# Performance work log

Measured on AMD Instinct MI355X. Metric: run time of the kernel, lower is better.

## Reference

```python
import jax, jax.numpy as jnp
import numpy as np

N, E = 100000, 1600000
IN_D, HID, OUT_D = 64, 64, 16
BN_EPS = 1e-5


def setup_inputs() -> dict:
    key = jax.random.key(0)
    ks = list(jax.random.split(key, 32))
    k = iter(ks)
    inp = {}
    inp["x"] = jax.random.normal(next(k), (N, IN_D), dtype=jnp.float32)
    inp["edge_index"] = jax.random.randint(next(k), (2, E), 0, N, dtype=jnp.int64)
    def lin(kk, fan_in, fan_out):
        s = 1.0 / np.sqrt(fan_in)
        return jax.random.uniform(kk, (fan_in, fan_out), jnp.float32, -s, s)
    for i, ind in ((1, IN_D), (2, HID), (3, HID)):
        inp[f"eps{i}"] = jnp.zeros((), jnp.float32)
        inp[f"w{i}1"] = lin(next(k), ind, HID)
        inp[f"b{i}1"] = jnp.zeros((HID,), jnp.float32)
        inp[f"w{i}2"] = lin(next(k), HID, HID)
        inp[f"b{i}2"] = jnp.zeros((HID,), jnp.float32)
        inp[f"g{i}"] = jnp.ones((HID,), jnp.float32)
        inp[f"bt{i}"] = jnp.zeros((HID,), jnp.float32)
    inp["wl"] = lin(next(k), HID, OUT_D)
    inp["bl"] = jnp.zeros((OUT_D,), jnp.float32)
    return inp


def _gin_conv(x, src, dst, eps, w1, b1, w2, b2, g, bt):
    # scatter-add neighbor sum: agg[i] = sum_{(s->i) in E} x[s]
    agg = jax.ops.segment_sum(x[src], dst, num_segments=N)
    h = (1.0 + eps) * x + agg
    h = jax.nn.relu(h @ w1 + b1)
    h = jax.nn.relu(h @ w2 + b2)
    # BatchNorm1d over nodes (training mode: batch stats, biased variance)
    mu = jnp.mean(h, axis=0)
    var = jnp.var(h, axis=0)
    h = (h - mu) * jax.lax.rsqrt(var + BN_EPS) * g + bt
    return h


def reference(x, edge_index,
              eps1, w11, b11, w12, b12, g1, bt1,
              eps2, w21, b21, w22, b22, g2, bt2,
              eps3, w31, b31, w32, b32, g3, bt3,
              wl, bl):
    src, dst = edge_index[0], edge_index[1]
    h = jax.nn.relu(_gin_conv(x, src, dst, eps1, w11, b11, w12, b12, g1, bt1))
    h = jax.nn.relu(_gin_conv(h, src, dst, eps2, w21, b21, w22, b22, g2, bt2))
    h = jax.nn.relu(_gin_conv(h, src, dst, eps3, w31, b31, w32, b32, g3, bt3))
    return h @ wl + bl
```

## Files before the change

kernel.cpp:

```cpp
#include <hip/hip_runtime.h>
#include <hip/hip_fp16.h>
#include <math.h>

#define N_NODES 100000
#define NC 391
#define NBLK64 1563
#define BN_EPS 1e-5f
#define PART_BLOCKS 128

typedef _Float16 half4v __attribute__((ext_vector_type(4)));
typedef float f32x4 __attribute__((ext_vector_type(4)));

__global__ void zero_misc_k(float* stats, int* gcnt) {
    int gid = blockIdx.x * blockDim.x + threadIdx.x;
    if (gid < 384) stats[gid] = 0.f;
    if (gid < NC) gcnt[gid] = 0;
}

__global__ void tofp16_k(const float* __restrict__ x, __half* __restrict__ xh, int n4) {
    int gid = blockIdx.x * blockDim.x + threadIdx.x;
    if (gid >= n4) return;
    float4 v = reinterpret_cast<const float4*>(x)[gid];
    union { float2 f; __half2 h[2]; } u;
    u.h[0] = __float22half2_rn(make_float2(v.x, v.y));
    u.h[1] = __float22half2_rn(make_float2(v.z, v.w));
    reinterpret_cast<float2*>(xh)[gid] = u.f;
}

__global__ void wtr_k(const float* w0, const float* w1, const float* w2,
                      const float* w3, const float* w4, const float* w5,
                      _Float16* wth) {
    const float* src[6] = {w0, w1, w2, w3, w4, w5};
    const float* W = src[blockIdx.x];
    _Float16* D = wth + (size_t)blockIdx.x * 4096;
    for (int idx = threadIdx.x; idx < 4096; idx += 256) {
        int k = idx >> 6, c = idx & 63;
        D[c * 64 + k] = (_Float16)W[idx];
    }
}

__global__ __launch_bounds__(256) void histC_k(const int* __restrict__ ei,
                                               int* __restrict__ gcnt, int E) {
    __shared__ int cnt[NC];
    for (int i = threadIdx.x; i < NC; i += 256) cnt[i] = 0;
    __syncthreads();
    int per = (E + gridDim.x - 1) / gridDim.x;
    int s0 = blockIdx.x * per, s1 = min(E, s0 + per);
    for (int e = s0 + threadIdx.x; e < s1; e += 256)
        atomicAdd(&cnt[ei[E + e] >> 8], 1);
    __syncthreads();
    for (int i = threadIdx.x; i < NC; i += 256)
        if (cnt[i]) atomicAdd(&gcnt[i], cnt[i]);
}

__global__ __launch_bounds__(256) void scanC_k(const int* __restrict__ gcnt,
                                               int* __restrict__ cbase,
                                               int* __restrict__ gcursor) {
    __shared__ int tmp[256];
    int t = threadIdx.x;
    int v0 = (2 * t < NC) ? gcnt[2 * t] : 0;
    int v1 = (2 * t + 1 < NC) ? gcnt[2 * t + 1] : 0;
    int s = v0 + v1;
    tmp[t] = s;
    __syncthreads();
    for (int off = 1; off < 256; off <<= 1) {
        int a = (t >= off) ? tmp[t - off] : 0;
        __syncthreads();
        tmp[t] += a;
        __syncthreads();
    }
    int run = tmp[t] - s;
    if (2 * t < NC) { cbase[2 * t] = run; gcursor[2 * t] = run; }
    run += v0;
    if (2 * t + 1 < NC) { cbase[2 * t + 1] = run; gcursor[2 * t + 1] = run; }
    if (t == 255) cbase[NC] = tmp[255];
}

__global__ __launch_bounds__(256) void partC_k(const int* __restrict__ ei,
                                               int* __restrict__ gcursor,
                                               int* __restrict__ part, int E) {
    __shared__ int cnt[NC];
    __shared__ int base[NC];
    for (int i = threadIdx.x; i < NC; i += 256) cnt[i] = 0;
    __syncthreads();
    int per = (E + gridDim.x - 1) / gridDim.x;
    int s0 = blockIdx.x * per, s1 = min(E, s0 + per);
    for (int e = s0 + threadIdx.x; e < s1; e += 256)
        atomicAdd(&cnt[ei[E + e] >> 8], 1);
    __syncthreads();
    for (int i = threadIdx.x; i < NC; i += 256) {
        int c = cnt[i];
        base[i] = c ? atomicAdd(&gcursor[i], c) : 0;
    }
    __syncthreads();
    for (int i = threadIdx.x; i < NC; i += 256) cnt[i] = 0;
    __syncthreads();
    for (int e = s0 + threadIdx.x; e < s1; e += 256) {
        int s = ei[e], d = ei[E + e];
        int b = d >> 8, dl = d & 255;
        int lo = atomicAdd(&cnt[b], 1);
        part[base[b] + lo] = (dl << 17) | s;
    }
}

__global__ __launch_bounds__(256) void csrD_k(const int* __restrict__ part,
                                              const int* __restrict__ cbase,
                                              int* __restrict__ row_ptr,
                                              int* __restrict__ csr_src) {
    __shared__ int cnt[256];
    __shared__ int tmp[256];
    __shared__ int cur[256];
    int b = blockIdx.x;
    int t = threadIdx.x;
    int e0 = cbase[b], e1 = cbase[b + 1];
    cnt[t] = 0;
    __syncthreads();
    for (int i = e0 + t; i < e1; i += 256) atomicAdd(&cnt[(part[i] >> 17) & 255], 1);
    __syncthreads();
    int c = cnt[t];
    tmp[t] = c;
    __syncthreads();
    for (int off = 1; off < 256; off <<= 1) {
        int a = (t >= off) ? tmp[t - off] : 0;
        __syncthreads();
        tmp[t] += a;
        __syncthreads();
    }
    int excl = tmp[t] - c;
    int node = b * 256 + t;
    if (node < N_NODES) row_ptr[node] = e0 + excl;
    cur[t] = e0 + excl;
    __syncthreads();
    for (int i = e0 + t; i < e1; i += 256) {
        int u = part[i];
        int dl = (u >> 17) & 255;
        int pos = atomicAdd(&cur[dl], 1);
        csr_src[pos] = u & 0x1FFFF;
    }
    if (b == NC - 1 && t == 0) row_ptr[N_NODES] = cbase[NC];
}

__global__ __launch_bounds__(512) void layer_k(
    const __half* __restrict__ hin,
    const int* __restrict__ row_ptr, const int* __restrict__ csr_src,
    const float* __restrict__ epsp,
    const _Float16* __restrict__ wt1, const float* __restrict__ b1,
    const _Float16* __restrict__ wt2, const float* __restrict__ b2,
    __half* __restrict__ hout, float* __restrict__ stats) {
    __shared__ _Float16 xs[64][72];
    __shared__ float sred[128];

    int tid = threadIdx.x;
    int r0 = blockIdx.x * 64;
    if (tid < 128) sred[tid] = 0.f;

    float eps1 = 1.0f + *epsp;
    int cg8 = tid & 7;
    int rloc = tid >> 3;
    union F4H { float4 f; __half2 h[4]; };

    {
        int node = r0 + rloc;
        float acc[8] = {0.f, 0.f, 0.f, 0.f, 0.f, 0.f, 0.f, 0.f};
        if (node < N_NODES) {
            F4H sv;
            sv.f = reinterpret_cast<const float4*>(hin + (size_t)node * 64)[cg8];
#pragma unroll
            for (int p = 0; p < 4; ++p) {
                float2 gg = __half22float2(sv.h[p]);
                acc[2 * p] = gg.x * eps1;
                acc[2 * p + 1] = gg.y * eps1;
            }
            int j0 = row_ptr[node], j1 = row_ptr[node + 1];
            int j = j0;
            for (; j + 8 <= j1; j += 8) {
                int idx[8];
#pragma unroll
                for (int q = 0; q < 8; ++q) idx[q] = csr_src[j + q];
                F4H u[8];
#pragma unroll
                for (int q = 0; q < 8; ++q)
                    u[q].f = reinterpret_cast<const float4*>(hin + (size_t)idx[q] * 64)[cg8];
#pragma unroll
                for (int q = 0; q < 8; ++q) {
#pragma unroll
                    for (int p = 0; p < 4; ++p) {
                        float2 gg = __half22float2(u[q].h[p]);
                        acc[2 * p] += gg.x;
                        acc[2 * p + 1] += gg.y;
                    }
                }
            }
            for (; j + 2 <= j1; j += 2) {
                int ia = csr_src[j], ib = csr_src[j + 1];
                F4H ua, ub;
                ua.f = reinterpret_cast<const float4*>(hin + (size_t)ia * 64)[cg8];
                ub.f = reinterpret_cast<const float4*>(hin + (size_t)ib * 64)[cg8];
#pragma unroll
                for (int p = 0; p < 4; ++p) {
                    float2 ga = __half22float2(ua.h[p]);
                    float2 gb = __half22float2(ub.h[p]);
                    acc[2 * p] += ga.x + gb.x;
                    acc[2 * p + 1] += ga.y + gb.y;
                }
            }
            for (; j < j1; ++j) {
                F4H u;
                u.f = reinterpret_cast<const float4*>(hin + (size_t)csr_src[j] * 64)[cg8];
#pragma unroll
                for (int p = 0; p < 4; ++p) {
                    float2 gg = __half22float2(u.h[p]);
                    acc[2 * p] += gg.x;
                    acc[2 * p + 1] += gg.y;
                }
            }
        }
        F4H o;
#pragma unroll
        for (int p = 0; p < 4; ++p)
            o.h[p] = __float22half2_rn(make_float2(acc[2 * p], acc[2 * p + 1]));
        *reinterpret_cast<float4*>(&xs[rloc][cg8 * 8]) = o.f;
    }
    __syncthreads();

    int wid = tid >> 6, l = tid & 63;
    int strip = wid & 3, half = wid >> 2;
    int c = l & 15, g = l >> 4;
    int r_base = r0 + strip * 16;

    half4v a1[4];
#pragma unroll
    for (int kk = 0; kk < 4; ++kk)
        a1[kk] = *reinterpret_cast<const half4v*>(&xs[strip * 16 + c][g * 4 + kk * 16]);

    f32x4 acc1[2];
#pragma unroll
    for (int nn = 0; nn < 2; ++nn) {
        int n = half * 2 + nn;
        const _Float16* bb = wt1 + (size_t)(n * 16 + c) * 64 + g * 4;
        half4v bf[4];
#pragma unroll
        for (int kk = 0; kk < 4; ++kk)
            bf[kk] = *reinterpret_cast<const half4v*>(bb + kk * 16);
        f32x4 z = {0.f, 0.f, 0.f, 0.f};
#pragma unroll
        for (int kk = 0; kk < 4; ++kk)
            z = __builtin_amdgcn_mfma_f32_16x16x16f16(a1[kk], bf[kk], z, 0, 0, 0);
        acc1[nn] = z;
    }
    __syncthreads();

#pragma unroll
    for (int nn = 0; nn < 2; ++nn) {
        int n = half * 2 + nn;
        float bj = b1[n * 16 + c];
#pragma unroll
        for (int e = 0; e < 4; ++e) {
            float v = fmaxf(acc1[nn][e] + bj, 0.f);
            xs[strip * 16 + g * 4 + e][n * 16 + c] = (_Float16)v;
        }
    }
    __syncthreads();

    half4v a2[4];
#pragma unroll
    for (int kk = 0; kk < 4; ++kk)
        a2[kk] = *reinterpret_cast<const half4v*>(&xs[strip * 16 + c][kk * 16 + g * 4]);

    f32x4 acc2[2];
#pragma unroll
    for (int nn = 0; nn < 2; ++nn) {
        int n = half * 2 + nn;
        const _Float16* bb = wt2 + (size_t)(n * 16 + c) * 64 + g * 4;
        half4v bf[4];
#pragma unroll
        for (int kk = 0; kk < 4; ++kk)
            bf[kk] = *reinterpret_cast<const half4v*>(bb + kk * 16);
        f32x4 z = {0.f, 0.f, 0.f, 0.f};
#pragma unroll
        for (int kk = 0; kk < 4; ++kk)
            z = __builtin_amdgcn_mfma_f32_16x16x16f16(a2[kk], bf[kk], z, 0, 0, 0);
        acc2[nn] = z;
    }
    __syncthreads();

#pragma unroll
    for (int nn = 0; nn < 2; ++nn) {
        int n = half * 2 + nn;
        float bj = b2[n * 16 + c];
        float s = 0.f, q = 0.f;
#pragma unroll
        for (int e = 0; e < 4; ++e) {
            float v = fmaxf(acc2[nn][e] + bj, 0.f);
            xs[strip * 16 + g * 4 + e][n * 16 + c] = (_Float16)v;
            if (r_base + g * 4 + e < N_NODES) { s += v; q += v * v; }
        }
        atomicAdd(&sred[n * 16 + c], s);
        atomicAdd(&sred[64 + n * 16 + c], q);
    }
    __syncthreads();

    {
        int row = wid * 8 + (l >> 3);
        int colh = (l & 7) * 8;
        int grow = r0 + row;
        if (grow < N_NODES) {
            float4 v = *reinterpret_cast<const float4*>(&xs[row][colh]);
            *reinterpret_cast<float4*>(reinterpret_cast<__half*>(hout) +
                                       (size_t)grow * 64 + colh) = v;
        }
    }

    if (tid < 128) atomicAdd(&stats[tid], sred[tid]);
}

__global__ __launch_bounds__(256) void bnrelu_k(const __half* hin,
                                                const float* __restrict__ stats,
                                                const float* __restrict__ g,
                                                const float* __restrict__ bt,
                                                __half* hout) {
    __shared__ float ssc[64], sof[64];
    int tid = threadIdx.x;
    if (tid < 64) {
        float mean = stats[tid] * (1.f / N_NODES);
        float var = stats[64 + tid] * (1.f / N_NODES) - mean * mean;
        float sc = g[tid] * rsqrtf(var + BN_EPS);
        ssc[tid] = sc;
        sof[tid] = bt[tid] - mean * sc;
    }
    __syncthreads();
    int gid = blockIdx.x * 256 + tid;
    if (gid >= N_NODES * 8) return;
    int c0 = (gid & 7) * 8;
    union { float4 f; __half2 h[4]; } u;
    u.f = reinterpret_cast<const float4*>(hin)[gid];
#pragma unroll
    for (int q = 0; q < 4; ++q) {
        float2 v = __half22float2(u.h[q]);
        v.x = fmaxf(fmaf(v.x, ssc[c0 + 2 * q], sof[c0 + 2 * q]), 0.f);
        v.y = fmaxf(fmaf(v.y, ssc[c0 + 2 * q + 1], sof[c0 + 2 * q + 1]), 0.f);
        u.h[q] = __float22half2_rn(v);
    }
    reinterpret_cast<float4*>(hout)[gid] = u.f;
}

__global__ __launch_bounds__(256) void final_k(const __half* __restrict__ hin,
                                               const float* __restrict__ wl,
                                               const float* __restrict__ bl,
                                               float* __restrict__ out) {
    __shared__ float xs[64][68];
    __shared__ float wsh[64 * 16];
    __shared__ float bsh[16];
    int tid = threadIdx.x;
    int r0 = blockIdx.x * 64;

    reinterpret_cast<float4*>(wsh)[tid] = reinterpret_cast<const float4*>(wl)[tid];
    if (tid < 16) bsh[tid] = bl[tid];

    {
        int rr = tid >> 4, cg = tid & 15;
#pragma unroll
        for (int i = 0; i < 4; ++i) {
            int r = rr + i * 16;
            float4 v = make_float4(0.f, 0.f, 0.f, 0.f);
            if (r0 + r < N_NODES) {
                union { float2 f; __half2 h[2]; } u;
                u.f = reinterpret_cast<const float2*>(hin + (size_t)(r0 + r) * 64)[cg];
                float2 f0 = __half22float2(u.h[0]);
                float2 f1 = __half22float2(u.h[1]);
                v = make_float4(f0.x, f0.y, f1.x, f1.y);
            }
            xs[cg * 4 + 0][r] = v.x;
            xs[cg * 4 + 1][r] = v.y;
            xs[cg * 4 + 2][r] = v.z;
            xs[cg * 4 + 3][r] = v.w;
        }
    }
    __syncthreads();

    int tc = tid & 3, r = tid >> 2;
    int c = tc * 4;
    float acc0 = 0.f, acc1 = 0.f, acc2 = 0.f, acc3 = 0.f;
#pragma unroll 8
    for (int k = 0; k < 64; ++k) {
        float xv = xs[k][r];
        float4 wv = *reinterpret_cast<const float4*>(&wsh[k * 16 + c]);
        acc0 = fmaf(xv, wv.x, acc0);
        acc1 = fmaf(xv, wv.y, acc1);
        acc2 = fmaf(xv, wv.z, acc2);
        acc3 = fmaf(xv, wv.w, acc3);
    }
    int row = r0 + r;
    if (row < N_NODES) {
        float4 o = make_float4(acc0 + bsh[c], acc1 + bsh[c + 1], acc2 + bsh[c + 2], acc3 + bsh[c + 3]);
        *reinterpret_cast<float4*>(out + (size_t)row * 16 + c) = o;
    }
}

extern "C" void kernel_launch(void* const* d_in, const int* in_sizes, int n_in,
                              void* d_out, int out_size, void* d_ws, size_t ws_size,
                              hipStream_t stream) {
    const float* x = (const float*)d_in[0];
    const int* ei = (const int*)d_in[1];
    const int E = in_sizes[1] / 2;

    const float* eps[3] = {(const float*)d_in[2], (const float*)d_in[9], (const float*)d_in[16]};
    const float* w1[3]  = {(const float*)d_in[3], (const float*)d_in[10], (const float*)d_in[17]};
    const float* b1[3]  = {(const float*)d_in[4], (const float*)d_in[11], (const float*)d_in[18]};
    const float* w2[3]  = {(const float*)d_in[5], (const float*)d_in[12], (const float*)d_in[19]};
    const float* b2[3]  = {(const float*)d_in[6], (const float*)d_in[13], (const float*)d_in[20]};
    const float* g[3]   = {(const float*)d_in[7], (const float*)d_in[14], (const float*)d_in[21]};
    const float* bt[3]  = {(const float*)d_in[8], (const float*)d_in[15], (const float*)d_in[22]};
    const float* wl = (const float*)d_in[23];
    const float* bl = (const float*)d_in[24];

    __half* xh   = (__half*)d_ws;
    __half* ha   = xh + (size_t)N_NODES * 64;
    __half* hb   = ha + (size_t)N_NODES * 64;
    _Float16* wth = (_Float16*)(hb + (size_t)N_NODES * 64);
    float* stats = (float*)(wth + 6 * 4096);
    int* gcnt    = (int*)(stats + 384);
    int* cbase   = gcnt + NC;
    int* gcursor = cbase + (NC + 1);
    int* row_ptr = gcursor + NC;
    int* tail    = row_ptr + (N_NODES + 1);
    size_t used  = (size_t)((char*)tail - (char*)d_ws);

    int* csr_src = tail;
    int* part;
    if (used + 2 * (size_t)E * 4 <= ws_size) {
        part = csr_src + E;
    } else {
        part = (int*)d_out;
    }

    const int n4 = N_NODES * 16;

    zero_misc_k<<<2, 256, 0, stream>>>(stats, gcnt);
    tofp16_k<<<(n4 + 255) / 256, 256, 0, stream>>>(x, xh, n4);
    wtr_k<<<6, 256, 0, stream>>>(w1[0], w2[0], w1[1], w2[1], w1[2], w2[2], wth);
    histC_k<<<PART_BLOCKS, 256, 0, stream>>>(ei, gcnt, E);
    scanC_k<<<1, 256, 0, stream>>>(gcnt, cbase, gcursor);
    partC_k<<<PART_BLOCKS, 256, 0, stream>>>(ei, gcursor, part, E);
    csrD_k<<<NC, 256, 0, stream>>>(part, cbase, row_ptr, csr_src);

    const int bnblk = (N_NODES * 8 + 255) / 256;

    layer_k<<<NBLK64, 512, 0, stream>>>(xh, row_ptr, csr_src, eps[0],
                                        wth + 0 * 4096, b1[0], wth + 1 * 4096, b2[0],
                                        ha, stats + 0);
    bnrelu_k<<<bnblk, 256, 0, stream>>>(ha, stats + 0, g[0], bt[0], ha);

    layer_k<<<NBLK64, 512, 0, stream>>>(ha, row_ptr, csr_src, eps[1],
                                        wth + 2 * 4096, b1[1], wth + 3 * 4096, b2[1],
                                        hb, stats + 128);
    bnrelu_k<<<bnblk, 256, 0, stream>>>(hb, stats + 128, g[1], bt[1], hb);

    layer_k<<<NBLK64, 512, 0, stream>>>(hb, row_ptr, csr_src, eps[2],
                                        wth + 4 * 4096, b1[2], wth + 5 * 4096, b2[2],
                                        ha, stats + 256);
    bnrelu_k<<<bnblk, 256, 0, stream>>>(ha, stats + 256, g[2], bt[2], ha);

    final_k<<<(N_NODES + 63) / 64, 256, 0, stream>>>(ha, wl, bl, (float*)d_out);
}
```

Measured before the change: 334.7 us.

## Bucket CSR edges by source range to improve neighbor gather locality

The edge partition now buckets by both a coarse source range (7 passes of 16384 nodes) and the destination chunk. Each CSR row therefore lists neighbors grouped by source region, which is meant to make the feature gathers in the three layer kernels more cache-friendly. In exchange, the histogram and partition kernels use a 7x larger shared histogram and also read source indices. The scan kernel adds a serial single-thread pass to compute per-chunk starts, and the CSR build loops over passes with extra barriers.

```diff
diff --git a/kernel.cpp b/kernel.cpp
--- a/kernel.cpp
+++ b/kernel.cpp
@@ -4,6 +4,9 @@
 
 #define N_NODES 100000
 #define NC 391
+#define NPASS 7
+#define SRC_SHIFT 14
+#define FLATC (NC * NPASS)
 #define NBLK64 1563
 #define BN_EPS 1e-5f
 #define PART_BLOCKS 128
@@ -14,7 +17,7 @@
 __global__ void zero_misc_k(float* stats, int* gcnt) {
     int gid = blockIdx.x * blockDim.x + threadIdx.x;
     if (gid < 384) stats[gid] = 0.f;
-    if (gid < NC) gcnt[gid] = 0;
+    if (gid < FLATC) gcnt[gid] = 0;
 }
 
 __global__ void tofp16_k(const float* __restrict__ x, __half* __restrict__ xh, int n4) {
@@ -41,26 +44,34 @@
 
 __global__ __launch_bounds__(256) void histC_k(const int* __restrict__ ei,
                                                int* __restrict__ gcnt, int E) {
-    __shared__ int cnt[NC];
-    for (int i = threadIdx.x; i < NC; i += 256) cnt[i] = 0;
+    __shared__ int cnt[FLATC];
+    for (int i = threadIdx.x; i < FLATC; i += 256) cnt[i] = 0;
     __syncthreads();
     int per = (E + gridDim.x - 1) / gridDim.x;
     int s0 = blockIdx.x * per, s1 = min(E, s0 + per);
-    for (int e = s0 + threadIdx.x; e < s1; e += 256)
-        atomicAdd(&cnt[ei[E + e] >> 8], 1);
-    __syncthreads();
-    for (int i = threadIdx.x; i < NC; i += 256)
+    for (int e = s0 + threadIdx.x; e < s1; e += 256) {
+        int s = ei[e], d = ei[E + e];
+        atomicAdd(&cnt[(s >> SRC_SHIFT) * NC + (d >> 8)], 1);
+    }
+    __syncthreads();
+    for (int i = threadIdx.x; i < FLATC; i += 256)
         if (cnt[i]) atomicAdd(&gcnt[i], cnt[i]);
 }
 
 __global__ __launch_bounds__(256) void scanC_k(const int* __restrict__ gcnt,
                                                int* __restrict__ cbase,
-                                               int* __restrict__ gcursor) {
+                                               int* __restrict__ gcursor,
+                                               int* __restrict__ bstart) {
     __shared__ int tmp[256];
     int t = threadIdx.x;
-    int v0 = (2 * t < NC) ? gcnt[2 * t] : 0;
-    int v1 = (2 * t + 1 < NC) ? gcnt[2 * t + 1] : 0;
-    int s = v0 + v1;
+    int v[11];
+    int s = 0;
+#pragma unroll
+    for (int j = 0; j < 11; ++j) {
+        int idx = t * 11 + j;
+        v[j] = (idx < FLATC) ? gcnt[idx] : 0;
+        s += v[j];
+    }
     tmp[t] = s;
     __syncthreads();
     for (int off = 1; off < 256; off <<= 1) {
@@ -70,41 +81,59 @@
         __syncthreads();
     }
     int run = tmp[t] - s;
-    if (2 * t < NC) { cbase[2 * t] = run; gcursor[2 * t] = run; }
-    run += v0;
-    if (2 * t + 1 < NC) { cbase[2 * t + 1] = run; gcursor[2 * t + 1] = run; }
-    if (t == 255) cbase[NC] = tmp[255];
+#pragma unroll
+    for (int j = 0; j < 11; ++j) {
+        int idx = t * 11 + j;
+        if (idx < FLATC) { cbase[idx] = run; gcursor[idx] = run; }
+        run += v[j];
+    }
+    if (t == 255) cbase[FLATC] = tmp[255];
+    __syncthreads();
+    if (t == 0) {
+        int run2 = 0;
+        for (int b = 0; b < NC; ++b) {
+            int tot = 0;
+            for (int p = 0; p < NPASS; ++p) tot += gcnt[p * NC + b];
+            bstart[b] = run2;
+            run2 += tot;
+        }
+        bstart[NC] = run2;
+    }
 }
 
 __global__ __launch_bounds__(256) void partC_k(const int* __restrict__ ei,
                                                int* __restrict__ gcursor,
                                                int* __restrict__ part, int E) {
-    __shared__ int cnt[NC];
-    __shared__ int base[NC];
-    for (int i = threadIdx.x; i < NC; i += 256) cnt[i] = 0;
+    __shared__ int cnt[FLATC];
+    __shared__ int base[FLATC];
+    for (int i = threadIdx.x; i < FLATC; i += 256) cnt[i] = 0;
     __syncthreads();
     int per = (E + gridDim.x - 1) / gridDim.x;
     int s0 = blockIdx.x * per, s1 = min(E, s0 + per);
-    for (int e = s0 + threadIdx.x; e < s1; e += 256)
-        atomicAdd(&cnt[ei[E + e] >> 8], 1);
-    __syncthreads();
-    for (int i = threadIdx.x; i < NC; i += 256) {
+    for (int e = s0 + threadIdx.x; e < s1; e += 256) {
+        int s = ei[e], d = ei[E + e];
+        atomicAdd(&cnt[(s >> SRC_SHIFT) * NC + (d >> 8)], 1);
+    }
+    __syncthreads();
+    for (int i = threadIdx.x; i < FLATC; i += 256) {
         int c = cnt[i];
         base[i] = c ? atomicAdd(&gcursor[i], c) : 0;
     }
     __syncthreads();
-    for (int i = threadIdx.x; i < NC; i += 256) cnt[i] = 0;
+    for (int i = threadIdx.x; i < FLATC; i += 256) cnt[i] = 0;
     __syncthreads();
     for (int e = s0 + threadIdx.x; e < s1; e += 256) {
         int s = ei[e], d = ei[E + e];
-        int b = d >> 8, dl = d & 255;
-        int lo = atomicAdd(&cnt[b], 1);
-        part[base[b] + lo] = (dl << 17) | s;
+        int key = (s >> SRC_SHIFT) * NC + (d >> 8);
+        int dl = d & 255;
+        int lo = atomicAdd(&cnt[key], 1);
+        part[base[key] + lo] = (dl << 17) | s;
     }
 }
 
 __global__ __launch_bounds__(256) void csrD_k(const int* __restrict__ part,
                                               const int* __restrict__ cbase,
+                                              const int* __restrict__ bstart,
                                               int* __restrict__ row_ptr,
                                               int* __restrict__ csr_src) {
     __shared__ int cnt[256];
@@ -112,10 +141,12 @@
     __shared__ int cur[256];
     int b = blockIdx.x;
     int t = threadIdx.x;
-    int e0 = cbase[b], e1 = cbase[b + 1];
     cnt[t] = 0;
     __syncthreads();
-    for (int i = e0 + t; i < e1; i += 256) atomicAdd(&cnt[(part[i] >> 17) & 255], 1);
+    for (int p = 0; p < NPASS; ++p) {
+        int e0 = cbase[p * NC + b], e1 = cbase[p * NC + b + 1];
+        for (int i = e0 + t; i < e1; i += 256) atomicAdd(&cnt[(part[i] >> 17) & 255], 1);
+    }
     __syncthreads();
     int c = cnt[t];
     tmp[t] = c;
@@ -128,16 +159,21 @@
     }
     int excl = tmp[t] - c;
     int node = b * 256 + t;
-    if (node < N_NODES) row_ptr[node] = e0 + excl;
-    cur[t] = e0 + excl;
-    __syncthreads();
-    for (int i = e0 + t; i < e1; i += 256) {
-        int u = part[i];
-        int dl = (u >> 17) & 255;
-        int pos = atomicAdd(&cur[dl], 1);
-        csr_src[pos] = u & 0x1FFFF;
-    }
-    if (b == NC - 1 && t == 0) row_ptr[N_NODES] = cbase[NC];
+    int b0 = bstart[b];
+    if (node < N_NODES) row_ptr[node] = b0 + excl;
+    cur[t] = b0 + excl;
+    __syncthreads();
+    for (int p = 0; p < NPASS; ++p) {
+        int e0 = cbase[p * NC + b], e1 = cbase[p * NC + b + 1];
+        for (int i = e0 + t; i < e1; i += 256) {
+            int u = part[i];
+            int dl = (u >> 17) & 255;
+            int pos = atomicAdd(&cur[dl], 1);
+            csr_src[pos] = u & 0x1FFFF;
+        }
+        __syncthreads();
+    }
+    if (b == NC - 1 && t == 0) row_ptr[N_NODES] = bstart[NC];
 }
 
 __global__ __launch_bounds__(512) void layer_k(
@@ -420,9 +456,10 @@
     _Float16* wth = (_Float16*)(hb + (size_t)N_NODES * 64);
     float* stats = (float*)(wth + 6 * 4096);
     int* gcnt    = (int*)(stats + 384);
-    int* cbase   = gcnt + NC;
-    int* gcursor = cbase + (NC + 1);
-    int* row_ptr = gcursor + NC;
+    int* cbase   = gcnt + FLATC;
+    int* gcursor = cbase + (FLATC + 1);
+    int* bstart  = gcursor + FLATC;
+    int* row_ptr = bstart + (NC + 1);
     int* tail    = row_ptr + (N_NODES + 1);
     size_t used  = (size_t)((char*)tail - (char*)d_ws);
 
@@ -436,13 +473,13 @@
 
     const int n4 = N_NODES * 16;
 
-    zero_misc_k<<<2, 256, 0, stream>>>(stats, gcnt);
+    zero_misc_k<<<(FLATC + 255) / 256, 256, 0, stream>>>(stats, gcnt);
     tofp16_k<<<(n4 + 255) / 256, 256, 0, stream>>>(x, xh, n4);
     wtr_k<<<6, 256, 0, stream>>>(w1[0], w2[0], w1[1], w2[1], w1[2], w2[2], wth);
     histC_k<<<PART_BLOCKS, 256, 0, stream>>>(ei, gcnt, E);
-    scanC_k<<<1, 256, 0, stream>>>(gcnt, cbase, gcursor);
+    scanC_k<<<1, 256, 0, stream>>>(gcnt, cbase, gcursor, bstart);
     partC_k<<<PART_BLOCKS, 256, 0, stream>>>(ei, gcursor, part, E);
-    csrD_k<<<NC, 256, 0, stream>>>(part, cbase, row_ptr, csr_src);
+    csrD_k<<<NC, 256, 0, stream>>>(part, cbase, bstart, row_ptr, csr_src);
 
     const int bnblk = (N_NODES * 8 + 255) / 256;
 
```

New measurement: 371.0 us. 10.9% more time.
